# Optimization experiments

Hardware: AMD Instinct MI355X
Metric: run time of the kernel (lower is better)

## Reference

```python
import jax, jax.numpy as jnp
import numpy as np

N = 1048576   # nodes (1024x1024 fluid grid)
E = 8388608   # edges (avg degree 8)
IDX_NODE_X, IDX_NODE_Y = 0, 1
IDX_EDGE_X, IDX_EDGE_Y = 0, 1


def setup_inputs() -> dict:
    key = jax.random.key(0)
    ks = jax.random.split(key, 9)
    v_x = jax.random.normal(ks[0], (N, 2), jnp.float32)
    v_prev_x = jax.random.normal(ks[1], (N, 2), jnp.float32)
    p_x = jax.random.normal(ks[2], (N, 1), jnp.float32)
    p_prev_x = jax.random.normal(ks[3], (N, 1), jnp.float32)
    rho_x = jax.random.normal(ks[4], (N, 1), jnp.float32)
    rho_prev_x = jax.random.normal(ks[5], (N, 1), jnp.float32)
    edge_attr = jax.random.normal(ks[6], (E, 2), jnp.float32)
    # mimic grid finite-difference sparsity: ~half the entries of each
    # direction column are exactly zero, exercising the != 0 edge masking
    keep = jax.random.bernoulli(ks[7], 0.5, (E, 2))
    edge_attr = jnp.where(keep, edge_attr, 0.0)
    edge_index = jax.random.randint(ks[8], (2, E), 0, N, dtype=jnp.int64)
    return dict(
        v_x=v_x, v_prev_x=v_prev_x, p_x=p_x, p_prev_x=p_prev_x,
        rho_x=rho_x, rho_prev_x=rho_prev_x,
        M=jnp.float32(1.0), eta=jnp.float32(1.0), zeta=jnp.float32(1.0),
        dt=jnp.float32(0.01), edge_attr=edge_attr, edge_index=edge_index,
    )


def _spatial_derivative(x, src, dst, edge_attr, mask, idx_node, idx_edge, n):
    """Gather-compute-scatter finite difference: scatter-mean of
    (x[dst, idx_node] - x[src, idx_node]) / edge_attr[:, idx_edge]
    over the masked edge subset, aggregated at the source node."""
    diff = x[dst, idx_node] - x[src, idx_node]                  # [E]
    denom = jnp.where(mask, edge_attr[:, idx_edge], 1.0)        # avoid /0 on masked-out edges
    contrib = jnp.where(mask, diff / denom, 0.0)                # [E]
    sums = jax.ops.segment_sum(contrib, src, num_segments=n)    # [N]
    cnt = jax.ops.segment_sum(mask.astype(x.dtype), src, num_segments=n)
    return sums / jnp.maximum(cnt, 1.0)                         # [N]


def reference(v_x, v_prev_x, p_x, p_prev_x, rho_x, rho_prev_x, M, eta, zeta, dt, edge_attr, edge_index):
    n = v_x.shape[0]
    src, dst = edge_index[0], edge_index[1]
    vp = v_x * p_x                                  # [N,2] * [N,1] -> [N,2]
    mask_x = edge_attr[:, IDX_NODE_X] != 0          # edges with x-offset
    mask_y = edge_attr[:, IDX_NODE_Y] != 0          # edges with y-offset
    d_x = _spatial_derivative(vp, src, dst, edge_attr, mask_x, IDX_NODE_X, IDX_EDGE_X, n)
    d_y = _spatial_derivative(vp, src, dst, edge_attr, mask_y, IDX_NODE_Y, IDX_EDGE_Y, n)
    loss_continuity = (d_x + d_y)[:, None] + (p_x - p_prev_x) / dt   # [N,1]
    return loss_continuity
```

## Files before the change

### kernel.cpp

```cpp
#include <hip/hip_runtime.h>


#define NPB      2048
#define NPB_LOG  11
#define NBUCK_MAX 512
#define CE       4096
#define CB       1024
#define EPT      4
#define CCAP     4608
#define MAXCHUNK 2048
#define K_OFF    1073741824.0


__global__ void node_pre_fast(const float2* __restrict__ v,
                              const float* __restrict__ p,
                              float2* __restrict__ vp,
                              double2* __restrict__ side, int N) {
    int i = blockIdx.x * blockDim.x + threadIdx.x;
    int stride = gridDim.x * blockDim.x;
    for (; i < N; i += stride) {
        float2 vi = v[i];
        float pi = p[i];
        vp[i] = make_float2(vi.x * pi, vi.y * pi);
        side[i] = make_double2(0.0, 0.0);
    }
}

__device__ __forceinline__ void route_rec(uint2 r, int k, size_t rb, int slot,
                                          uint2* __restrict__ recs,
                                          const float2* __restrict__ vp,
                                          double2* __restrict__ side) {
    if (slot < CCAP) { recs[rb + slot] = r; return; }
    unsigned sl = r.x & (NPB - 1u);
    bool diry = (r.x >> 11) & 1u;
    int d = (int)(r.x >> 12);
    float a = __uint_as_float(r.y);
    int s = k * NPB + (int)sl;
    float2 vpd = vp[d], vs = vp[s];
    float c = (diry ? vpd.y - vs.y : vpd.x - vs.x) / a;
    unsafeAtomicAdd(diry ? &side[s].y : &side[s].x, (double)c + K_OFF);
}

__global__ __launch_bounds__(CB) void chunk_sort(
        const float2* __restrict__ ea,
        const int* __restrict__ src_idx,
        const int* __restrict__ dst_idx,
        const float2* __restrict__ vp,
        uint2* __restrict__ recs,
        int* __restrict__ off_mat,
        int* __restrict__ cnt_mat,
        double2* __restrict__ side,
        int nbuck, int E) {
    __shared__ uint2 stage[CCAP];
    __shared__ int hist[NBUCK_MAX];
    __shared__ int tl[NBUCK_MAX];
    __shared__ int cur[NBUCK_MAX];
    int c = blockIdx.x, t = threadIdx.x;
    int e0 = c * CE;

    uint2 R0[EPT], R1[EPT];
    int K[EPT], NR[EPT];
#pragma unroll
    for (int i = 0; i < EPT; ++i) {
        int e = e0 + i * CB + t;
        NR[i] = 0; K[i] = 0;
        if (e < E) {
            float2 a = ea[e];
            bool mx = (a.x != 0.f);
            bool my = (a.y != 0.f);
            if (mx || my) {
                int s = src_idx[e];
                int d = dst_idx[e];
                K[i] = s >> NPB_LOG;
                unsigned sl = (unsigned)(s & (NPB - 1));
                unsigned dm = (unsigned)d << 12;
                NR[i] = (int)mx + (int)my;
                uint2 rx = make_uint2(sl | dm, __float_as_uint(a.x));
                uint2 ry = make_uint2(sl | 0x800u | dm, __float_as_uint(a.y));
                R0[i] = mx ? rx : ry;
                R1[i] = ry;
            }
        }
    }
    if (t < nbuck) hist[t] = 0;
    __syncthreads();
#pragma unroll
    for (int i = 0; i < EPT; ++i)
        if (NR[i]) atomicAdd(&hist[K[i]], NR[i]);
    __syncthreads();
    if (t < nbuck) tl[t] = hist[t];
    __syncthreads();
    for (int off = 1; off < NBUCK_MAX; off <<= 1) {
        int x = 0;
        if (t < nbuck && t >= off) x = tl[t - off];
        __syncthreads();
        if (t < nbuck) tl[t] += x;
        __syncthreads();
    }
    int total = tl[nbuck - 1];
    if (t < nbuck) {
        int excl = tl[t] - hist[t];
        cur[t] = excl;
        off_mat[(size_t)c * nbuck + t] = excl;
        cnt_mat[(size_t)c * nbuck + t] = hist[t];
    }
    __syncthreads();
    size_t rb = (size_t)c * CCAP;
    if (total <= CCAP) {
#pragma unroll
        for (int i = 0; i < EPT; ++i)
            if (NR[i]) {
                int slot = atomicAdd(&cur[K[i]], NR[i]);
                stage[slot] = R0[i];
                if (NR[i] == 2) stage[slot + 1] = R1[i];
            }
        __syncthreads();
        for (int j = t; j < total; j += CB) recs[rb + j] = stage[j];
    } else {
#pragma unroll
        for (int i = 0; i < EPT; ++i)
            if (NR[i]) {
                int slot = atomicAdd(&cur[K[i]], NR[i]);
                route_rec(R0[i], K[i], rb, slot, recs, vp, side);
                if (NR[i] == 2) route_rec(R1[i], K[i], rb, slot + 1, recs, vp, side);
            }
    }
}

__global__ __launch_bounds__(1024) void bucket_reduce(
        const uint2* __restrict__ recs,
        const int* __restrict__ off_mat,
        const int* __restrict__ cnt_mat,
        const float2* __restrict__ vp,
        const double2* __restrict__ side,
        const float* __restrict__ p,
        const float* __restrict__ p_prev,
        const float* __restrict__ dt_ptr,
        float* __restrict__ out,
        int nchunk, int nbuck, int N) {
    __shared__ float2 vps[NPB];
    __shared__ double2 acc[NPB];
    __shared__ int glen[MAXCHUNK];
    __shared__ int goff[MAXCHUNK];
    int k = blockIdx.x, t = threadIdx.x;
    int g0 = k * NPB;
    for (int i = t; i < NPB; i += 1024) {
        int g = g0 + i;
        vps[i] = (g < N) ? vp[g] : make_float2(0.f, 0.f);
        acc[i] = make_double2(0.0, 0.0);
    }
    for (int c = t; c < MAXCHUNK; c += 1024) {
        int len = 0, off = 0;
        if (c < nchunk) {
            off = off_mat[(size_t)c * nbuck + k];
            int cnt = cnt_mat[(size_t)c * nbuck + k];
            len = min(cnt, max(0, CCAP - off));
        }
        goff[c] = off;
        glen[c] = len;
    }
    __syncthreads();
    for (int off = 1; off < MAXCHUNK; off <<= 1) {
        int i0 = t, i1 = t + 1024;
        int x0 = (i0 >= off) ? glen[i0 - off] : 0;
        int x1 = (i1 >= off) ? glen[i1 - off] : 0;
        __syncthreads();
        glen[i0] += x0;
        glen[i1] += x1;
        __syncthreads();
    }
    int total = glen[MAXCHUNK - 1];
    for (int idx = t; idx < total; idx += 1024) {
        int lo = 0, hi = nchunk - 1;
        while (lo < hi) {
            int mid = (lo + hi) >> 1;
            if (glen[mid] > idx) hi = mid; else lo = mid + 1;
        }
        int pre = lo ? glen[lo - 1] : 0;
        uint2 r = recs[(size_t)lo * CCAP + goff[lo] + (idx - pre)];
        unsigned sl = r.x & (NPB - 1u);
        bool diry = (r.x >> 11) & 1u;
        int d = (int)(r.x >> 12);
        float a = __uint_as_float(r.y);
        float2 vpd = vp[d];
        float2 vs = vps[sl];
        float c = (diry ? vpd.y - vs.y : vpd.x - vs.x) / a;
        unsafeAtomicAdd(diry ? &acc[sl].y : &acc[sl].x, (double)c + K_OFF);
    }
    __syncthreads();
    float inv_dt = 1.0f / dt_ptr[0];
    for (int i = t; i < NPB; i += 1024) {
        int g = g0 + i;
        if (g < N) {
            double2 A = acc[i];
            double2 S = side[g];
            double Ax = A.x + S.x, Ay = A.y + S.y;
            double cx = rint(Ax * (1.0 / K_OFF));
            double sx = Ax - cx * K_OFF;
            double cy = rint(Ay * (1.0 / K_OFF));
            double sy = Ay - cy * K_OFF;
            out[g] = (float)(sx / fmax(cx, 1.0)) + (float)(sy / fmax(cy, 1.0))
                   + (p[g] - p_prev[g]) * inv_dt;
        }
    }
}


__global__ void fb_node_pre(const float2* __restrict__ v,
                            const float* __restrict__ p,
                            float2* __restrict__ vp,
                            double2* __restrict__ acc, int N) {
    int i = blockIdx.x * blockDim.x + threadIdx.x;
    int stride = gridDim.x * blockDim.x;
    for (; i < N; i += stride) {
        float2 vi = v[i];
        float pi = p[i];
        vp[i] = make_float2(vi.x * pi, vi.y * pi);
        acc[i] = make_double2(0.0, 0.0);
    }
}

__global__ void fb_edge_scatter(const float2* __restrict__ vp,
                                const float2* __restrict__ ea,
                                const int* __restrict__ src_idx,
                                const int* __restrict__ dst_idx,
                                double2* __restrict__ acc, int E) {
    int e = blockIdx.x * blockDim.x + threadIdx.x;
    if (e >= E) return;
    float2 a = ea[e];
    bool mx = (a.x != 0.f);
    bool my = (a.y != 0.f);
    if (!mx && !my) return;
    int s = src_idx[e];
    int d = dst_idx[e];
    float2 vs = vp[s];
    float2 vd = vp[d];
    double* basep = (double*)&acc[s];
    if (mx) unsafeAtomicAdd(basep + 0, (double)((vd.x - vs.x) / a.x) + K_OFF);
    if (my) unsafeAtomicAdd(basep + 1, (double)((vd.y - vs.y) / a.y) + K_OFF);
}

__global__ void fb_node_final(const double2* __restrict__ acc,
                              const float* __restrict__ p,
                              const float* __restrict__ p_prev,
                              const float* __restrict__ dt_ptr,
                              float* __restrict__ out, int N) {
    int i = blockIdx.x * blockDim.x + threadIdx.x;
    int stride = gridDim.x * blockDim.x;
    float inv_dt = 1.0f / dt_ptr[0];
    for (; i < N; i += stride) {
        double2 A = acc[i];
        double cx = rint(A.x * (1.0 / K_OFF));
        double sx = A.x - cx * K_OFF;
        double cy = rint(A.y * (1.0 / K_OFF));
        double sy = A.y - cy * K_OFF;
        out[i] = (float)(sx / fmax(cx, 1.0)) + (float)(sy / fmax(cy, 1.0))
               + (p[i] - p_prev[i]) * inv_dt;
    }
}


extern "C" void kernel_launch(void* const* d_in, const int* in_sizes, int n_in,
                              void* d_out, int out_size, void* d_ws, size_t ws_size,
                              hipStream_t stream) {
    const float2* v_x    = (const float2*)d_in[0];
    const float*  p_x    = (const float*)d_in[2];
    const float*  p_prev = (const float*)d_in[3];
    const float*  dt     = (const float*)d_in[9];
    const float2* ea     = (const float2*)d_in[10];
    const int*    eidx   = (const int*)d_in[11];

    const int N = in_sizes[2];
    const int E = in_sizes[10] / 2;
    const int* src_idx = eidx;
    const int* dst_idx = eidx + E;

    const int nbuck  = (N + NPB - 1) >> NPB_LOG;
    const int nchunk = (E + CE - 1) / CE;

    char* w = (char*)d_ws;
    float2*  vp      = (float2*)w;    w += (size_t)N * sizeof(float2);
    double2* side    = (double2*)w;   w += (size_t)N * sizeof(double2);
    int*     off_mat = (int*)w;       w += (size_t)nchunk * nbuck * sizeof(int);
    int*     cnt_mat = (int*)w;       w += (size_t)nchunk * nbuck * sizeof(int);
    w = (char*)(((uintptr_t)w + 15) & ~(uintptr_t)15);
    uint2*   recs    = (uint2*)w;     w += (size_t)nchunk * CCAP * sizeof(uint2);
    size_t need_fast = (size_t)(w - (char*)d_ws);

    if (nbuck <= NBUCK_MAX && nchunk <= MAXCHUNK && N <= (1 << 20)
        && ws_size >= need_fast) {
        node_pre_fast<<<2048, 256, 0, stream>>>(v_x, p_x, vp, side, N);
        chunk_sort<<<nchunk, CB, 0, stream>>>(ea, src_idx, dst_idx, vp, recs,
                                              off_mat, cnt_mat, side, nbuck, E);
        bucket_reduce<<<nbuck, 1024, 0, stream>>>(recs, off_mat, cnt_mat, vp,
                                                  side, p_x, p_prev, dt,
                                                  (float*)d_out, nchunk, nbuck, N);
    } else {
        float2*  fvp  = (float2*)d_ws;
        double2* facc = (double2*)((char*)d_ws + (size_t)N * sizeof(float2));
        fb_node_pre<<<2048, 256, 0, stream>>>(v_x, p_x, fvp, facc, N);
        fb_edge_scatter<<<(E + 255) / 256, 256, 0, stream>>>(
            fvp, ea, src_idx, dst_idx, facc, E);
        fb_node_final<<<2048, 256, 0, stream>>>(
            facc, p_x, p_prev, dt, (float*)d_out, N);
    }
}
```

Measured before the change: 162.5 us.

## Split x/y records into separate buckets with SoA node values and u16 offsets

Sorts x-direction and y-direction edge records into separate bucket keys so that bucket_reduce handles them in two phases, each gathering only a single float component (vpx or vpy) from structure-of-arrays buffers. The per-chunk offset and count matrices shrink to 16-bit entries, and a global overflow flag lets the final pass skip reading the side array when no chunk overflowed. The aim is to cut gather bytes per edge and metadata traffic. The cost is a second scan over the chunk metadata per bucket and twice as many histogram keys.

```diff
diff --git a/kernel.cpp b/kernel.cpp
--- a/kernel.cpp
+++ b/kernel.cpp
@@ -4,6 +4,7 @@
 #define NPB      2048
 #define NPB_LOG  11
 #define NBUCK_MAX 512
+#define NKEY_MAX 1024
 #define CE       4096
 #define CB       1024
 #define EPT      4
@@ -14,56 +15,65 @@
 
 __global__ void node_pre_fast(const float2* __restrict__ v,
                               const float* __restrict__ p,
-                              float2* __restrict__ vp,
-                              double2* __restrict__ side, int N) {
+                              float* __restrict__ vpx,
+                              float* __restrict__ vpy,
+                              double2* __restrict__ side,
+                              int* __restrict__ oflow, int N) {
     int i = blockIdx.x * blockDim.x + threadIdx.x;
     int stride = gridDim.x * blockDim.x;
     for (; i < N; i += stride) {
         float2 vi = v[i];
         float pi = p[i];
-        vp[i] = make_float2(vi.x * pi, vi.y * pi);
+        vpx[i] = vi.x * pi;
+        vpy[i] = vi.y * pi;
         side[i] = make_double2(0.0, 0.0);
     }
-}
-
-__device__ __forceinline__ void route_rec(uint2 r, int k, size_t rb, int slot,
+    if (blockIdx.x == 0 && threadIdx.x == 0) *oflow = 0;
+}
+
+__device__ __forceinline__ void route_rec(unsigned meta, unsigned abits,
+                                          bool diry, int k, size_t rb, int slot,
                                           uint2* __restrict__ recs,
-                                          const float2* __restrict__ vp,
-                                          double2* __restrict__ side) {
-    if (slot < CCAP) { recs[rb + slot] = r; return; }
-    unsigned sl = r.x & (NPB - 1u);
-    bool diry = (r.x >> 11) & 1u;
-    int d = (int)(r.x >> 12);
-    float a = __uint_as_float(r.y);
-    int s = k * NPB + (int)sl;
-    float2 vpd = vp[d], vs = vp[s];
-    float c = (diry ? vpd.y - vs.y : vpd.x - vs.x) / a;
+                                          const float* __restrict__ vpx,
+                                          const float* __restrict__ vpy,
+                                          double2* __restrict__ side,
+                                          int* __restrict__ oflow) {
+    if (slot < CCAP) { recs[rb + slot] = make_uint2(meta, abits); return; }
+    int sl = (int)(meta & (NPB - 1u));
+    int d = (int)(meta >> 12);
+    int s = k * NPB + sl;
+    float a = __uint_as_float(abits);
+    float c = ((diry ? vpy[d] : vpx[d]) - (diry ? vpy[s] : vpx[s])) / a;
     unsafeAtomicAdd(diry ? &side[s].y : &side[s].x, (double)c + K_OFF);
+    atomicOr(oflow, 1);
 }
 
 __global__ __launch_bounds__(CB) void chunk_sort(
         const float2* __restrict__ ea,
         const int* __restrict__ src_idx,
         const int* __restrict__ dst_idx,
-        const float2* __restrict__ vp,
+        const float* __restrict__ vpx,
+        const float* __restrict__ vpy,
         uint2* __restrict__ recs,
-        int* __restrict__ off_mat,
-        int* __restrict__ cnt_mat,
+        unsigned short* __restrict__ off_mat,
+        unsigned short* __restrict__ cnt_mat,
         double2* __restrict__ side,
+        int* __restrict__ oflow,
         int nbuck, int E) {
     __shared__ uint2 stage[CCAP];
-    __shared__ int hist[NBUCK_MAX];
-    __shared__ int tl[NBUCK_MAX];
-    __shared__ int cur[NBUCK_MAX];
+    __shared__ int hist[NKEY_MAX];
+    __shared__ int tl[NKEY_MAX];
+    __shared__ int cur[NKEY_MAX];
     int c = blockIdx.x, t = threadIdx.x;
+    int nkey = 2 * nbuck;
     int e0 = c * CE;
 
-    uint2 R0[EPT], R1[EPT];
-    int K[EPT], NR[EPT];
+    unsigned M[EPT], AX[EPT], AY[EPT];
+    int K[EPT], FL[EPT];
 #pragma unroll
     for (int i = 0; i < EPT; ++i) {
         int e = e0 + i * CB + t;
-        NR[i] = 0; K[i] = 0;
+        FL[i] = 0; K[i] = 0;
         if (e < E) {
             float2 a = ea[e];
             bool mx = (a.x != 0.f);
@@ -72,120 +82,141 @@
                 int s = src_idx[e];
                 int d = dst_idx[e];
                 K[i] = s >> NPB_LOG;
-                unsigned sl = (unsigned)(s & (NPB - 1));
-                unsigned dm = (unsigned)d << 12;
-                NR[i] = (int)mx + (int)my;
-                uint2 rx = make_uint2(sl | dm, __float_as_uint(a.x));
-                uint2 ry = make_uint2(sl | 0x800u | dm, __float_as_uint(a.y));
-                R0[i] = mx ? rx : ry;
-                R1[i] = ry;
-            }
-        }
-    }
-    if (t < nbuck) hist[t] = 0;
+                M[i] = (unsigned)(s & (NPB - 1)) | ((unsigned)d << 12);
+                AX[i] = __float_as_uint(a.x);
+                AY[i] = __float_as_uint(a.y);
+                FL[i] = (int)mx | ((int)my << 1);
+            }
+        }
+    }
+    if (t < nkey) hist[t] = 0;
     __syncthreads();
 #pragma unroll
-    for (int i = 0; i < EPT; ++i)
-        if (NR[i]) atomicAdd(&hist[K[i]], NR[i]);
-    __syncthreads();
-    if (t < nbuck) tl[t] = hist[t];
-    __syncthreads();
-    for (int off = 1; off < NBUCK_MAX; off <<= 1) {
+    for (int i = 0; i < EPT; ++i) {
+        if (FL[i] & 1) atomicAdd(&hist[K[i]], 1);
+        if (FL[i] & 2) atomicAdd(&hist[nbuck + K[i]], 1);
+    }
+    __syncthreads();
+    if (t < nkey) tl[t] = hist[t];
+    __syncthreads();
+    for (int off = 1; off < nkey; off <<= 1) {
         int x = 0;
-        if (t < nbuck && t >= off) x = tl[t - off];
-        __syncthreads();
-        if (t < nbuck) tl[t] += x;
-        __syncthreads();
-    }
-    int total = tl[nbuck - 1];
-    if (t < nbuck) {
+        if (t < nkey && t >= off) x = tl[t - off];
+        __syncthreads();
+        if (t < nkey) tl[t] += x;
+        __syncthreads();
+    }
+    int total = tl[nkey - 1];
+    if (t < nkey) {
         int excl = tl[t] - hist[t];
         cur[t] = excl;
-        off_mat[(size_t)c * nbuck + t] = excl;
-        cnt_mat[(size_t)c * nbuck + t] = hist[t];
+        off_mat[(size_t)c * nkey + t] = (unsigned short)excl;
+        cnt_mat[(size_t)c * nkey + t] = (unsigned short)hist[t];
     }
     __syncthreads();
     size_t rb = (size_t)c * CCAP;
     if (total <= CCAP) {
 #pragma unroll
-        for (int i = 0; i < EPT; ++i)
-            if (NR[i]) {
-                int slot = atomicAdd(&cur[K[i]], NR[i]);
-                stage[slot] = R0[i];
-                if (NR[i] == 2) stage[slot + 1] = R1[i];
-            }
+        for (int i = 0; i < EPT; ++i) {
+            if (FL[i] & 1) {
+                int slot = atomicAdd(&cur[K[i]], 1);
+                stage[slot] = make_uint2(M[i], AX[i]);
+            }
+            if (FL[i] & 2) {
+                int slot = atomicAdd(&cur[nbuck + K[i]], 1);
+                stage[slot] = make_uint2(M[i], AY[i]);
+            }
+        }
         __syncthreads();
         for (int j = t; j < total; j += CB) recs[rb + j] = stage[j];
     } else {
 #pragma unroll
-        for (int i = 0; i < EPT; ++i)
-            if (NR[i]) {
-                int slot = atomicAdd(&cur[K[i]], NR[i]);
-                route_rec(R0[i], K[i], rb, slot, recs, vp, side);
-                if (NR[i] == 2) route_rec(R1[i], K[i], rb, slot + 1, recs, vp, side);
-            }
+        for (int i = 0; i < EPT; ++i) {
+            if (FL[i] & 1) {
+                int slot = atomicAdd(&cur[K[i]], 1);
+                route_rec(M[i], AX[i], false, K[i], rb, slot, recs, vpx, vpy, side, oflow);
+            }
+            if (FL[i] & 2) {
+                int slot = atomicAdd(&cur[nbuck + K[i]], 1);
+                route_rec(M[i], AY[i], true, K[i], rb, slot, recs, vpx, vpy, side, oflow);
+            }
+        }
     }
 }
 
 __global__ __launch_bounds__(1024) void bucket_reduce(
         const uint2* __restrict__ recs,
-        const int* __restrict__ off_mat,
-        const int* __restrict__ cnt_mat,
-        const float2* __restrict__ vp,
+        const unsigned short* __restrict__ off_mat,
+        const unsigned short* __restrict__ cnt_mat,
+        const float* __restrict__ vpx,
+        const float* __restrict__ vpy,
         const double2* __restrict__ side,
+        const int* __restrict__ oflow,
         const float* __restrict__ p,
         const float* __restrict__ p_prev,
         const float* __restrict__ dt_ptr,
         float* __restrict__ out,
         int nchunk, int nbuck, int N) {
-    __shared__ float2 vps[NPB];
+    __shared__ float vpsx[NPB];
+    __shared__ float vpsy[NPB];
     __shared__ double2 acc[NPB];
     __shared__ int glen[MAXCHUNK];
     __shared__ int goff[MAXCHUNK];
+    __shared__ int s_of;
     int k = blockIdx.x, t = threadIdx.x;
     int g0 = k * NPB;
+    int nkey = 2 * nbuck;
     for (int i = t; i < NPB; i += 1024) {
         int g = g0 + i;
-        vps[i] = (g < N) ? vp[g] : make_float2(0.f, 0.f);
+        vpsx[i] = (g < N) ? vpx[g] : 0.f;
+        vpsy[i] = (g < N) ? vpy[g] : 0.f;
         acc[i] = make_double2(0.0, 0.0);
     }
-    for (int c = t; c < MAXCHUNK; c += 1024) {
-        int len = 0, off = 0;
-        if (c < nchunk) {
-            off = off_mat[(size_t)c * nbuck + k];
-            int cnt = cnt_mat[(size_t)c * nbuck + k];
-            len = min(cnt, max(0, CCAP - off));
-        }
-        goff[c] = off;
-        glen[c] = len;
-    }
-    __syncthreads();
-    for (int off = 1; off < MAXCHUNK; off <<= 1) {
-        int i0 = t, i1 = t + 1024;
-        int x0 = (i0 >= off) ? glen[i0 - off] : 0;
-        int x1 = (i1 >= off) ? glen[i1 - off] : 0;
-        __syncthreads();
-        glen[i0] += x0;
-        glen[i1] += x1;
-        __syncthreads();
-    }
-    int total = glen[MAXCHUNK - 1];
-    for (int idx = t; idx < total; idx += 1024) {
-        int lo = 0, hi = nchunk - 1;
-        while (lo < hi) {
-            int mid = (lo + hi) >> 1;
-            if (glen[mid] > idx) hi = mid; else lo = mid + 1;
-        }
-        int pre = lo ? glen[lo - 1] : 0;
-        uint2 r = recs[(size_t)lo * CCAP + goff[lo] + (idx - pre)];
-        unsigned sl = r.x & (NPB - 1u);
-        bool diry = (r.x >> 11) & 1u;
-        int d = (int)(r.x >> 12);
-        float a = __uint_as_float(r.y);
-        float2 vpd = vp[d];
-        float2 vs = vps[sl];
-        float c = (diry ? vpd.y - vs.y : vpd.x - vs.x) / a;
-        unsafeAtomicAdd(diry ? &acc[sl].y : &acc[sl].x, (double)c + K_OFF);
+    if (t == 0) s_of = *oflow;
+
+    for (int phase = 0; phase < 2; ++phase) {
+        int key = phase * nbuck + k;
+        __syncthreads();
+        for (int c = t; c < MAXCHUNK; c += 1024) {
+            int len = 0, off = 0;
+            if (c < nchunk) {
+                off = off_mat[(size_t)c * nkey + key];
+                int cnt = cnt_mat[(size_t)c * nkey + key];
+                len = min(cnt, max(0, CCAP - off));
+            }
+            goff[c] = off;
+            glen[c] = len;
+        }
+        __syncthreads();
+        for (int off = 1; off < MAXCHUNK; off <<= 1) {
+            int i0 = t, i1 = t + 1024;
+            int x0 = (i0 >= off) ? glen[i0 - off] : 0;
+            int x1 = glen[i1 - off];
+            __syncthreads();
+            glen[i0] += x0;
+            glen[i1] += x1;
+            __syncthreads();
+        }
+        int total = glen[MAXCHUNK - 1];
+        for (int idx = t; idx < total; idx += 1024) {
+            int lo = 0, hi = nchunk - 1;
+            while (lo < hi) {
+                int mid = (lo + hi) >> 1;
+                if (glen[mid] > idx) hi = mid; else lo = mid + 1;
+            }
+            int pre = lo ? glen[lo - 1] : 0;
+            uint2 r = recs[(size_t)lo * CCAP + goff[lo] + (idx - pre)];
+            int sl = (int)(r.x & (NPB - 1u));
+            int d = (int)(r.x >> 12);
+            float a = __uint_as_float(r.y);
+            if (phase == 0) {
+                float c = (vpx[d] - vpsx[sl]) / a;
+                unsafeAtomicAdd(&acc[sl].x, (double)c + K_OFF);
+            } else {
+                float c = (vpy[d] - vpsy[sl]) / a;
+                unsafeAtomicAdd(&acc[sl].y, (double)c + K_OFF);
+            }
+        }
     }
     __syncthreads();
     float inv_dt = 1.0f / dt_ptr[0];
@@ -193,12 +224,14 @@
         int g = g0 + i;
         if (g < N) {
             double2 A = acc[i];
-            double2 S = side[g];
-            double Ax = A.x + S.x, Ay = A.y + S.y;
-            double cx = rint(Ax * (1.0 / K_OFF));
-            double sx = Ax - cx * K_OFF;
-            double cy = rint(Ay * (1.0 / K_OFF));
-            double sy = Ay - cy * K_OFF;
+            if (s_of) {
+                double2 S = side[g];
+                A.x += S.x; A.y += S.y;
+            }
+            double cx = rint(A.x * (1.0 / K_OFF));
+            double sx = A.x - cx * K_OFF;
+            double cy = rint(A.y * (1.0 / K_OFF));
+            double sy = A.y - cy * K_OFF;
             out[g] = (float)(sx / fmax(cx, 1.0)) + (float)(sy / fmax(cy, 1.0))
                    + (p[g] - p_prev[g]) * inv_dt;
         }
@@ -277,23 +310,28 @@
 
     const int nbuck  = (N + NPB - 1) >> NPB_LOG;
     const int nchunk = (E + CE - 1) / CE;
+    const int nkey   = 2 * nbuck;
 
     char* w = (char*)d_ws;
-    float2*  vp      = (float2*)w;    w += (size_t)N * sizeof(float2);
+    float*   vpx     = (float*)w;     w += (size_t)N * sizeof(float);
+    float*   vpy     = (float*)w;     w += (size_t)N * sizeof(float);
     double2* side    = (double2*)w;   w += (size_t)N * sizeof(double2);
-    int*     off_mat = (int*)w;       w += (size_t)nchunk * nbuck * sizeof(int);
-    int*     cnt_mat = (int*)w;       w += (size_t)nchunk * nbuck * sizeof(int);
+    int*     oflow   = (int*)w;       w += 16;
+    unsigned short* off_mat = (unsigned short*)w;  w += (size_t)nchunk * nkey * sizeof(unsigned short);
+    unsigned short* cnt_mat = (unsigned short*)w;  w += (size_t)nchunk * nkey * sizeof(unsigned short);
     w = (char*)(((uintptr_t)w + 15) & ~(uintptr_t)15);
     uint2*   recs    = (uint2*)w;     w += (size_t)nchunk * CCAP * sizeof(uint2);
     size_t need_fast = (size_t)(w - (char*)d_ws);
 
     if (nbuck <= NBUCK_MAX && nchunk <= MAXCHUNK && N <= (1 << 20)
         && ws_size >= need_fast) {
-        node_pre_fast<<<2048, 256, 0, stream>>>(v_x, p_x, vp, side, N);
-        chunk_sort<<<nchunk, CB, 0, stream>>>(ea, src_idx, dst_idx, vp, recs,
-                                              off_mat, cnt_mat, side, nbuck, E);
-        bucket_reduce<<<nbuck, 1024, 0, stream>>>(recs, off_mat, cnt_mat, vp,
-                                                  side, p_x, p_prev, dt,
+        node_pre_fast<<<2048, 256, 0, stream>>>(v_x, p_x, vpx, vpy, side, oflow, N);
+        chunk_sort<<<nchunk, CB, 0, stream>>>(ea, src_idx, dst_idx, vpx, vpy,
+                                              recs, off_mat, cnt_mat, side,
+                                              oflow, nbuck, E);
+        bucket_reduce<<<nbuck, 1024, 0, stream>>>(recs, off_mat, cnt_mat,
+                                                  vpx, vpy, side, oflow,
+                                                  p_x, p_prev, dt,
                                                   (float*)d_out, nchunk, nbuck, N);
     } else {
         float2*  fvp  = (float2*)d_ws;
```

Result: slower. 177.4 us (+9.2%).
